# Performance work log

Hardware: AMD Instinct MI355X
Metric: run time of the kernel (lower is better)

## Reference

```python
import jax, jax.numpy as jnp
import numpy as np

MARGIN = 1.0
CONTR_LAMDA = 100.0
GN_LAMDA = 0.3
IMG_SCALE = 2
EPS = 1e-9


def bilinear(fmap, pts):
    # fmap: (B,C,H,W); pts: (B,N,2) as (x,y). Returns (B*N, C).
    B, C, H, W = fmap.shape
    N = pts.shape[1]
    x = jnp.clip(pts[..., 0], 0.0, W - 1.0)
    y = jnp.clip(pts[..., 1], 0.0, H - 1.0)
    x0 = jnp.floor(x)
    y0 = jnp.floor(y)
    wx = (x - x0)[:, None, :]
    wy = (y - y0)[:, None, :]
    x0i = x0.astype(jnp.int32)
    y0i = y0.astype(jnp.int32)
    x1i = jnp.minimum(x0i + 1, W - 1)
    y1i = jnp.minimum(y0i + 1, H - 1)
    fm = fmap.reshape(B, C, H * W)

    def gather(yi, xi):
        idx = yi * W + xi  # (B,N)
        idx = jnp.broadcast_to(idx[:, None, :], (B, C, N))
        return jnp.take_along_axis(fm, idx, axis=2)  # (B,C,N)

    v = (gather(y0i, x0i) * (1 - wx) * (1 - wy)
         + gather(y0i, x1i) * wx * (1 - wy)
         + gather(y1i, x0i) * (1 - wx) * wy
         + gather(y1i, x1i) * wx * wy)
    return v.transpose(0, 2, 1).reshape(B * N, C)


def grad2d(f):
    # central differences with edge replication (torch_gradient)
    fx = jnp.pad(f, ((0, 0), (0, 0), (0, 0), (1, 1)), mode='edge')
    gx = 0.5 * (fx[..., 2:] - fx[..., :-2])
    fy = jnp.pad(f, ((0, 0), (0, 0), (1, 1), (0, 0)), mode='edge')
    gy = 0.5 * (fy[..., 2:, :] - fy[..., :-2, :])
    return gx, gy


def gn_loss(f_t, fb, ub, noise):
    # f_t: (B*N,C); fb: (B,C,H,W); ub,noise: (B,N,2)
    B, N, _ = ub.shape
    xs = noise + ub
    f_s = bilinear(fb, xs)
    r = f_s - f_t  # (BN, C) residual
    gx, gy = grad2d(fb)
    Jx = bilinear(gx, xs)  # (BN, C)
    Jy = bilinear(gy, xs)
    # H = J^T J + eps*I  -- closed-form batched 2x2
    a = jnp.sum(Jx * Jx, axis=1) + EPS
    d = jnp.sum(Jy * Jy, axis=1) + EPS
    b = jnp.sum(Jx * Jy, axis=1)
    det = a * d - b * b
    bx = jnp.sum(Jx * r, axis=1)
    by = jnp.sum(Jy * r, axis=1)
    # Hinv @ (J^T r)
    ix = (d * bx - b * by) / det
    iy = (-b * bx + a * by) / det
    miu = xs.reshape(B * N, 2) - jnp.stack([ix, iy], axis=-1)
    du = ub.reshape(B * N, 2) - miu
    q = a * du[:, 0] ** 2 + 2.0 * b * du[:, 0] * du[:, 1] + d * du[:, 1] ** 2
    e1 = 0.5 * jnp.sum(q)
    e2 = B * N * jnp.log(jnp.asarray(2.0 * np.pi, jnp.float32)) - 0.5 * jnp.sum(jnp.log(det))
    return e1 + 2.0 * e2 / 7.0


def triplet_loss(fa_map, fb_map, ma, mb, ng):
    fa = bilinear(fa_map, ma)
    fp = bilinear(fb_map, mb)
    fn = bilinear(fb_map, ng)
    dp = jnp.linalg.norm(fa - fp, axis=1)
    dn = jnp.linalg.norm(fa - fn, axis=1)
    return jnp.mean(jax.nn.relu(dp - dn + MARGIN))


def setup_inputs() -> dict:
    key = jax.random.key(0)
    ks = jax.random.split(key, 16)
    B, C, N = 4, 32, 2048
    sizes = [64, 128, 256, 512]
    d = {}
    for i, h in enumerate(sizes):
        d[f'fa{i}'] = jax.random.normal(ks[i], (B, C, h, h), jnp.float32)
        d[f'fb{i}'] = jax.random.normal(ks[4 + i], (B, C, h, h), jnp.float32)
        d[f'noise{i}'] = jax.random.normal(ks[8 + i], (B, N, 2), jnp.float32)
    d['ma'] = jax.random.uniform(ks[12], (B, N, 2), jnp.float32) * 1024.0
    d['mb'] = jax.random.uniform(ks[13], (B, N, 2), jnp.float32) * 1024.0
    d['neg'] = jax.random.uniform(ks[14], (B, N, 2), jnp.float32) * 1024.0
    d['epoch'] = 5
    return d


def reference(fa0, fa1, fa2, fa3, fb0, fb1, fb2, fb3,
              noise0, noise1, noise2, noise3, ma, mb, neg, epoch):
    Fa = [fa0, fa1, fa2, fa3]
    Fb = [fb0, fb1, fb2, fb3]
    noises = [noise0, noise1, noise2, noise3]
    loss = jnp.float32(0.0)
    tl = jnp.float32(0.0)
    gl = jnp.float32(0.0)
    for i in range(4):
        level = 2 ** (3 - i)
        s = float(level * IMG_SCALE)
        f_t = bilinear(Fa[i], ma / s)
        lt = triplet_loss(Fa[i], Fb[i], ma / s, mb / s, neg / s)
        lg = gn_loss(f_t, Fb[i], mb / s, noises[i])
        loss = loss + CONTR_LAMDA * lt + GN_LAMDA * lg
        tl = tl + CONTR_LAMDA * lt
        gl = gl + GN_LAMDA * lg
    return loss, tl, gl
```

## Files before the change

kernel.cpp:

```cpp
#include <hip/hip_runtime.h>
#include <math.h>


struct BL { int x0, x1, y0, y1; float wx, wy; };
struct LevelPtrs { const float* fa[4]; const float* fb[4]; const float* nz[4]; };

__device__ __forceinline__ float2 load2u(const float* p) { float2 v; __builtin_memcpy(&v, p, 8); return v; }
__device__ __forceinline__ float4 load4u(const float* p) { float4 v; __builtin_memcpy(&v, p, 16); return v; }

__device__ __forceinline__ BL bl_setup2(float px, float py, int W, int H) {
    BL r;
    float x = fminf(fmaxf(px, 0.0f), (float)(W - 1));
    float y = fminf(fmaxf(py, 0.0f), (float)(H - 1));
    float fx = floorf(x), fy = floorf(y);
    r.wx = x - fx; r.wy = y - fy;
    r.x0 = (int)fx; r.y0 = (int)fy;
    if (r.x0 >= W - 1) { r.x0 = W - 2; r.wx = 1.0f; }
    if (r.y0 >= H - 1) { r.y0 = H - 2; r.wy = 1.0f; }
    r.x1 = r.x0 + 1;
    r.y1 = r.y0 + 1;
    return r;
}

__device__ __forceinline__ float bl_eval_slow(const float* __restrict__ f, int W, const BL& s) {
    float v00 = f[s.y0 * W + s.x0];
    float v01 = f[s.y0 * W + s.x1];
    float v10 = f[s.y1 * W + s.x0];
    float v11 = f[s.y1 * W + s.x1];
    float a0 = v00 + s.wx * (v01 - v00);
    float a1 = v10 + s.wx * (v11 - v10);
    return a0 + s.wy * (a1 - a0);
}

__device__ __forceinline__ void j_eval_slow(const float* __restrict__ f, int W, int H,
                                            const BL& s, float& Jx, float& Jy) {
    int xR0 = min(s.x0 + 1, W - 1), xL0 = max(s.x0 - 1, 0);
    int xR1 = min(s.x1 + 1, W - 1), xL1 = max(s.x1 - 1, 0);
    int yD0 = min(s.y0 + 1, H - 1), yU0 = max(s.y0 - 1, 0);
    int yD1 = min(s.y1 + 1, H - 1), yU1 = max(s.y1 - 1, 0);
    const float* r0 = f + s.y0 * W;
    const float* r1 = f + s.y1 * W;
    float gx00 = r0[xR0] - r0[xL0];
    float gx01 = r0[xR1] - r0[xL1];
    float gx10 = r1[xR0] - r1[xL0];
    float gx11 = r1[xR1] - r1[xL1];
    float gy00 = f[yD0 * W + s.x0] - f[yU0 * W + s.x0];
    float gy01 = f[yD0 * W + s.x1] - f[yU0 * W + s.x1];
    float gy10 = f[yD1 * W + s.x0] - f[yU1 * W + s.x0];
    float gy11 = f[yD1 * W + s.x1] - f[yU1 * W + s.x1];
    float g0 = gx00 + s.wx * (gx01 - gx00);
    float g1 = gx10 + s.wx * (gx11 - gx10);
    Jx = 0.5f * (g0 + s.wy * (g1 - g0));
    float h0 = gy00 + s.wx * (gy01 - gy00);
    float h1 = gy10 + s.wx * (gy11 - gy10);
    Jy = 0.5f * (h0 + s.wy * (h1 - h0));
}

__device__ __forceinline__ float wave64_sum(float v) {
    v += __shfl_xor(v, 32);
    v += __shfl_xor(v, 16);
    v += __shfl_xor(v, 8);
    v += __shfl_xor(v, 4);
    v += __shfl_xor(v, 2);
    v += __shfl_xor(v, 1);
    return v;
}

__device__ __forceinline__ float warp32_sum(float v) {
    v += __shfl_xor(v, 16);
    v += __shfl_xor(v, 8);
    v += __shfl_xor(v, 4);
    v += __shfl_xor(v, 2);
    v += __shfl_xor(v, 1);
    return v;
}

__global__ __launch_bounds__(1024) void sort3_kernel(
    const float* __restrict__ ma, const float* __restrict__ mb,
    const float* __restrict__ ng, int* __restrict__ perm) {
    const int cid = blockIdx.x >> 2;
    const int b = blockIdx.x & 3;
    const float* coords = (cid == 0) ? ma : (cid == 1) ? mb : ng;
    __shared__ unsigned int keys[2048];
    const float* cb = coords + (size_t)b * 2048 * 2;
    for (int i = threadIdx.x; i < 2048; i += 1024) {
        int ix = min(max((int)cb[i * 2 + 0], 0), 1023);
        int iy = min(max((int)cb[i * 2 + 1], 0), 1023);
        unsigned m = 0;
        #pragma unroll
        for (int t = 0; t < 10; ++t)
            m |= (((unsigned)(ix >> t) & 1u) << (2 * t)) | (((unsigned)(iy >> t) & 1u) << (2 * t + 1));
        keys[i] = (m << 11) | (unsigned)i;
    }
    __syncthreads();
    for (unsigned k = 2; k <= 2048; k <<= 1) {
        for (unsigned j = k >> 1; j > 0; j >>= 1) {
            unsigned t = threadIdx.x;
            unsigned i1 = 2 * t - (t & (j - 1));
            unsigned i2 = i1 + j;
            bool up = ((i1 & k) == 0);
            unsigned a = keys[i1], c = keys[i2];
            if ((a > c) == up) { keys[i1] = c; keys[i2] = a; }
            __syncthreads();
        }
    }
    for (int i = threadIdx.x; i < 2048; i += 1024)
        perm[cid * 8192 + b * 2048 + i] = (int)(keys[i] & 2047u);
}

__global__ __launch_bounds__(256) void gather_pass_kernel(
    LevelPtrs P, const float* __restrict__ ma, const float* __restrict__ ng,
    const int* __restrict__ perm, float* __restrict__ ft, float* __restrict__ fn) {
    const int bid = blockIdx.x;
    const int role = bid & 1;
    const int rest = bid >> 1;
    const int lvl = 3 - (rest >> 9);
    const int sub = rest & 511;
    const int g = sub >> 2;
    const int cq = sub & 3;
    const int tid = threadIdx.x;
    const int lane = tid & 63, w = tid >> 6;
    const int ch0 = cq * 8 + w * 2;
    const int rank = g * 64 + lane;
    const int b = rank >> 11;
    const int* pm = perm + (role ? 2 * 8192 : 0);
    const int q = (b << 11) + pm[rank];
    const int H = 64 << lvl, W = H, HW = H * W;
    const float inv_s = 0.0625f * (float)(1 << lvl);
    const float* coords = role ? ng : ma;
    const float px = coords[q * 2] * inv_s, py = coords[q * 2 + 1] * inv_s;
    BL s = bl_setup2(px, py, W, H);
    const float* src = role ? P.fb[lvl] : P.fa[lvl];
    const float* p0 = src + (size_t)(b * 32 + ch0) * HW + s.y0 * W + s.x0;
    const float* p1 = p0 + HW;

    float2 a0 = load2u(p0);
    float2 a1 = load2u(p0 + W);
    float2 c0 = load2u(p1);
    float2 c1 = load2u(p1 + W);
    __builtin_amdgcn_sched_barrier(0);
    float t0 = a0.x + s.wx * (a0.y - a0.x);
    float t1 = a1.x + s.wx * (a1.y - a1.x);
    float o0 = t0 + s.wy * (t1 - t0);
    float u0 = c0.x + s.wx * (c0.y - c0.x);
    float u1 = c1.x + s.wx * (c1.y - c1.x);
    float o1 = u0 + s.wy * (u1 - u0);

    float* dst = (role ? fn : ft) + ((size_t)lvl * 8192 + q) * 32 + ch0;
    float2 o = {o0, o1};
    *(float2*)dst = o;
}

__device__ __forceinline__ void consume_ch(
    const float* __restrict__ plane, int W, int H, const BL& sb, const BL& sx,
    bool interior, float2 m0, float2 m1,
    float4 r0, float4 r1, float4 r2, float4 r3,
    float ftv, float fnv,
    float& sp, float& sn, float& aa, float& dd, float& bb, float& bx, float& by) {
    float t0 = m0.x + sb.wx * (m0.y - m0.x);
    float t1 = m1.x + sb.wx * (m1.y - m1.x);
    float fpv = t0 + sb.wy * (t1 - t0);
    float fsv, Jx, Jy;
    if (interior) {
        float wx = sx.wx, wy = sx.wy;
        float a0 = r1.y + wx * (r1.z - r1.y);
        float a1 = r2.y + wx * (r2.z - r2.y);
        fsv = a0 + wy * (a1 - a0);
        float gx00 = r1.z - r1.x, gx01 = r1.w - r1.y;
        float gx10 = r2.z - r2.x, gx11 = r2.w - r2.y;
        float gy00 = r2.y - r0.y, gy01 = r2.z - r0.z;
        float gy10 = r3.y - r1.y, gy11 = r3.z - r1.z;
        float g0 = gx00 + wx * (gx01 - gx00);
        float g1 = gx10 + wx * (gx11 - gx10);
        Jx = 0.5f * (g0 + wy * (g1 - g0));
        float h0 = gy00 + wx * (gy01 - gy00);
        float h1 = gy10 + wx * (gy11 - gy10);
        Jy = 0.5f * (h0 + wy * (h1 - h0));
    } else {
        fsv = bl_eval_slow(plane, W, sx);
        j_eval_slow(plane, W, H, sx, Jx, Jy);
    }
    float rr = fsv - ftv;
    float dp = ftv - fpv, dn = ftv - fnv;
    sp += dp * dp;
    sn += dn * dn;
    aa += Jx * Jx;
    dd += Jy * Jy;
    bb += Jx * Jy;
    bx += Jx * rr;
    by += Jy * rr;
}

__global__ __launch_bounds__(256) void gn_main_kernel(
    LevelPtrs P, const float* __restrict__ mb, const int* __restrict__ perm_mb,
    const float* __restrict__ ft, const float* __restrict__ fn,
    float* __restrict__ blk_out) {
    const int bid = blockIdx.x;
    const int lvl = 3 - (bid >> 7);
    const int g = bid & 127;
    const int tid = threadIdx.x;
    const int lane = tid & 63, w = tid >> 6, ch0 = w * 8;
    const int rank = g * 64 + lane;
    const int b = rank >> 11;
    const int q = (b << 11) + perm_mb[rank];
    const int H = 64 << lvl, W = H, HW = H * W;
    const float inv_s = 0.0625f * (float)(1 << lvl);
    const float* noise = P.nz[lvl];
    const int p2 = q * 2;
    const float nzx = noise[p2], nzy = noise[p2 + 1];
    const float pbx = mb[p2] * inv_s, pby = mb[p2 + 1] * inv_s;
    const float xsx = nzx + pbx, xsy = nzy + pby;
    BL sb = bl_setup2(pbx, pby, W, H);
    BL sx = bl_setup2(xsx, xsy, W, H);
    const bool interior = (sx.x0 >= 1) & (sx.x0 <= W - 3) & (sx.y0 >= 1) & (sx.y0 <= H - 3);
    const int pbx0 = min(max(sx.x0 - 1, 0), W - 4);
    const int pby0 = min(max(sx.y0 - 1, 0), H - 4);
    const float* fb0 = P.fb[lvl] + (size_t)(b * 32 + ch0) * HW;

    const float* ftp = ft + ((size_t)lvl * 8192 + q) * 32 + ch0;
    const float* fnp = fn + ((size_t)lvl * 8192 + q) * 32 + ch0;
    float4 ftA = *(const float4*)ftp, ftB = *(const float4*)(ftp + 4);
    float4 fnA = *(const float4*)fnp, fnB = *(const float4*)(fnp + 4);
    float ftv[8] = {ftA.x, ftA.y, ftA.z, ftA.w, ftB.x, ftB.y, ftB.z, ftB.w};
    float fnv[8] = {fnA.x, fnA.y, fnA.z, fnA.w, fnB.x, fnB.y, fnB.z, fnB.w};

    float sp = 0, sn = 0, aa = 0, dd = 0, bb = 0, bx = 0, by = 0;
    const int mboff0 = sb.y0 * W + sb.x0;
    const int pboff = pby0 * W + pbx0;
    #pragma unroll
    for (int cc = 0; cc < 8; cc += 2) {
        const float* p0 = fb0 + (size_t)cc * HW;
        const float* p1 = p0 + HW;
        float2 m00 = load2u(p0 + mboff0);
        float2 m01 = load2u(p0 + mboff0 + W);
        float2 m10 = load2u(p1 + mboff0);
        float2 m11 = load2u(p1 + mboff0 + W);
        const float* xb0 = p0 + pboff;
        const float* xb1 = p1 + pboff;
        float4 r00 = load4u(xb0), r01 = load4u(xb0 + W), r02 = load4u(xb0 + 2 * W), r03 = load4u(xb0 + 3 * W);
        float4 r10 = load4u(xb1), r11 = load4u(xb1 + W), r12 = load4u(xb1 + 2 * W), r13 = load4u(xb1 + 3 * W);
        consume_ch(p0, W, H, sb, sx, interior, m00, m01, r00, r01, r02, r03,
                   ftv[cc], fnv[cc], sp, sn, aa, dd, bb, bx, by);
        consume_ch(p1, W, H, sb, sx, interior, m10, m11, r10, r11, r12, r13,
                   ftv[cc + 1], fnv[cc + 1], sp, sn, aa, dd, bb, bx, by);
    }

    __shared__ float red[4][64][7];
    red[w][lane][0] = sp; red[w][lane][1] = sn; red[w][lane][2] = aa;
    red[w][lane][3] = dd; red[w][lane][4] = bb; red[w][lane][5] = bx;
    red[w][lane][6] = by;
    __syncthreads();
    if (tid < 64) {
        float t[7];
        #pragma unroll
        for (int k = 0; k < 7; ++k)
            t[k] = red[0][tid][k] + red[1][tid][k] + red[2][tid][k] + red[3][tid][k];
        float a2 = t[2] + 1e-9f, d2 = t[3] + 1e-9f, b2 = t[4];
        float det = a2 * d2 - b2 * b2;
        float ix = (d2 * t[5] - b2 * t[6]) / det;
        float iy = (a2 * t[6] - b2 * t[5]) / det;
        float dux = ix - nzx;
        float duy = iy - nzy;
        float qv = a2 * dux * dux + 2.0f * b2 * dux * duy + d2 * duy * duy;
        float trip = fmaxf(sqrtf(t[0]) - sqrtf(t[1]) + 1.0f, 0.0f);
        float ld = logf(det);
        trip = wave64_sum(trip);
        qv = wave64_sum(qv);
        ld = wave64_sum(ld);
        if (tid == 0) {
            blk_out[bid * 3 + 0] = trip;
            blk_out[bid * 3 + 1] = qv;
            blk_out[bid * 3 + 2] = ld;
        }
    }
}

__global__ __launch_bounds__(256) void gn_final_kernel(
    const float* __restrict__ part, int nblk, float* __restrict__ out) {
    __shared__ double sd[3][256];
    double st = 0.0, sq = 0.0, sl = 0.0;
    for (int i = threadIdx.x; i < nblk; i += 256) {
        st += (double)part[i * 3 + 0];
        sq += (double)part[i * 3 + 1];
        sl += (double)part[i * 3 + 2];
    }
    sd[0][threadIdx.x] = st; sd[1][threadIdx.x] = sq; sd[2][threadIdx.x] = sl;
    __syncthreads();
    for (int s = 128; s > 0; s >>= 1) {
        if (threadIdx.x < s) {
            sd[0][threadIdx.x] += sd[0][threadIdx.x + s];
            sd[1][threadIdx.x] += sd[1][threadIdx.x + s];
            sd[2][threadIdx.x] += sd[2][threadIdx.x + s];
        }
        __syncthreads();
    }
    if (threadIdx.x == 0) {
        double S_t = sd[0][0], S_q = sd[1][0], S_l = sd[2][0];
        double tl = 100.0 * S_t / 8192.0;
        double e2 = 4.0 * 8192.0 * 1.8378770664093453 - 0.5 * S_l;
        double gl = 0.3 * (0.5 * S_q + (2.0 / 7.0) * e2);
        out[0] = (float)(tl + gl);
        out[1] = (float)tl;
        out[2] = (float)gl;
    }
}

struct Task {
    const float* fac;
    const float* fbc;
    BL sa, sb, sg, sx;
    float nzx, nzy;
    bool fast;
    float2 va0, va1, vb0, vb1, vg0, vg1;
    float4 xm, x0, x1, x2;
    float fav, fpv, fnv, fsv, Jx, Jy;
};

__device__ __forceinline__ void task_setup(Task& T, int rank, const LevelPtrs& P,
                                           int lvl, int c, int W, int H, float inv_s,
                                           const float* __restrict__ ma,
                                           const float* __restrict__ mb,
                                           const float* __restrict__ ng) {
    const int b = rank >> 11;
    const int q = rank;
    const int HW = H * W;
    T.fac = P.fa[lvl] + (size_t)(b * 32 + c) * HW;
    T.fbc = P.fb[lvl] + (size_t)(b * 32 + c) * HW;
    const float* noise = P.nz[lvl];
    const int p2 = q * 2;
    T.nzx = noise[p2]; T.nzy = noise[p2 + 1];
    const float pax = ma[p2] * inv_s, pay = ma[p2 + 1] * inv_s;
    const float pbx = mb[p2] * inv_s, pby = mb[p2 + 1] * inv_s;
    const float pnx = ng[p2] * inv_s, pny = ng[p2 + 1] * inv_s;
    const float xsx = T.nzx + pbx, xsy = T.nzy + pby;
    T.sa = bl_setup2(pax, pay, W, H);
    T.sb = bl_setup2(pbx, pby, W, H);
    T.sg = bl_setup2(pnx, pny, W, H);
    T.sx = bl_setup2(xsx, xsy, W, H);
    T.fast = (T.sx.x0 >= 1) & (T.sx.x0 <= W - 3) & (T.sx.y0 >= 1) & (T.sx.y0 <= H - 3);
}

__device__ __forceinline__ void task_issue(Task& T, int W, int H) {
    T.va0 = load2u(T.fac + T.sa.y0 * W + T.sa.x0);
    T.va1 = load2u(T.fac + T.sa.y1 * W + T.sa.x0);
    T.vb0 = load2u(T.fbc + T.sb.y0 * W + T.sb.x0);
    T.vb1 = load2u(T.fbc + T.sb.y1 * W + T.sb.x0);
    T.vg0 = load2u(T.fbc + T.sg.y0 * W + T.sg.x0);
    T.vg1 = load2u(T.fbc + T.sg.y1 * W + T.sg.x0);
    int bx0 = min(max(T.sx.x0 - 1, 0), W - 4);
    int by0 = min(max(T.sx.y0 - 1, 0), H - 4);
    const float* xbp = T.fbc + by0 * W + bx0;
    T.xm = load4u(xbp);
    T.x0 = load4u(xbp + W);
    T.x1 = load4u(xbp + 2 * W);
    T.x2 = load4u(xbp + 3 * W);
}

__device__ __forceinline__ void task_consume(Task& T, int W, int H) {
    {
        float t0 = T.va0.x + T.sa.wx * (T.va0.y - T.va0.x);
        float t1 = T.va1.x + T.sa.wx * (T.va1.y - T.va1.x);
        T.fav = t0 + T.sa.wy * (t1 - t0);
    }
    {
        float t0 = T.vb0.x + T.sb.wx * (T.vb0.y - T.vb0.x);
        float t1 = T.vb1.x + T.sb.wx * (T.vb1.y - T.vb1.x);
        T.fpv = t0 + T.sb.wy * (t1 - t0);
    }
    {
        float t0 = T.vg0.x + T.sg.wx * (T.vg0.y - T.vg0.x);
        float t1 = T.vg1.x + T.sg.wx * (T.vg1.y - T.vg1.x);
        T.fnv = t0 + T.sg.wy * (t1 - t0);
    }
    if (T.fast) {
        float wx = T.sx.wx, wy = T.sx.wy;
        float t0 = T.x0.y + wx * (T.x0.z - T.x0.y);
        float t1 = T.x1.y + wx * (T.x1.z - T.x1.y);
        T.fsv = t0 + wy * (t1 - t0);
        float gx00 = T.x0.z - T.x0.x, gx01 = T.x0.w - T.x0.y;
        float gx10 = T.x1.z - T.x1.x, gx11 = T.x1.w - T.x1.y;
        float gy00 = T.x1.y - T.xm.y, gy01 = T.x1.z - T.xm.z;
        float gy10 = T.x2.y - T.x0.y, gy11 = T.x2.z - T.x0.z;
        float g0 = gx00 + wx * (gx01 - gx00);
        float g1 = gx10 + wx * (gx11 - gx10);
        T.Jx = 0.5f * (g0 + wy * (g1 - g0));
        float h0 = gy00 + wx * (gy01 - gy00);
        float h1 = gy10 + wx * (gy11 - gy10);
        T.Jy = 0.5f * (h0 + wy * (h1 - h0));
    } else {
        T.fsv = bl_eval_slow(T.fbc, W, T.sx);
        j_eval_slow(T.fbc, W, H, T.sx, T.Jx, T.Jy);
    }
}

__device__ __forceinline__ void task_reduce(const Task& T, int c, float* red0,
                                            float* red1, float* red2, int slot2) {
    float r = T.fsv - T.fav;
    float a  = warp32_sum(T.Jx * T.Jx);
    float dd = warp32_sum(T.Jy * T.Jy);
    float bb = warp32_sum(T.Jx * T.Jy);
    float bx = warp32_sum(T.Jx * r);
    float by = warp32_sum(T.Jy * r);
    float dfp = T.fav - T.fpv, dfn = T.fav - T.fnv;
    float sp = warp32_sum(dfp * dfp);
    float sn = warp32_sum(dfn * dfn);
    if (c == 0) {
        a += 1e-9f; dd += 1e-9f;
        float det = a * dd - bb * bb;
        float ix = (dd * bx - bb * by) / det;
        float iy = (a * by - bb * bx) / det;
        float dux = ix - T.nzx;
        float duy = iy - T.nzy;
        float qv = a * dux * dux + 2.0f * bb * dux * duy + dd * duy * duy;
        red0[slot2] = fmaxf(sqrtf(sp) - sqrtf(sn) + 1.0f, 0.0f);
        red1[slot2] = qv;
        red2[slot2] = logf(det);
    }
}

__global__ __launch_bounds__(256) void gn_fallback_kernel(
    LevelPtrs P, const float* __restrict__ ma, const float* __restrict__ mb,
    const float* __restrict__ ng, float* __restrict__ blk_out) {
    const int tid = threadIdx.x;
    const int c = tid & 31;
    const int slot = tid >> 5;
    const int lvl = slot >> 1;
    const int po = slot & 1;
    const int bid = blockIdx.x;
    const int base = bid * 4;
    const int H = 64 << lvl;
    const int W = H;
    const float inv_s = 0.0625f * (float)(1 << lvl);

    Task T0, T1;
    task_setup(T0, base + po,     P, lvl, c, W, H, inv_s, ma, mb, ng);
    task_setup(T1, base + 2 + po, P, lvl, c, W, H, inv_s, ma, mb, ng);
    task_issue(T0, W, H);
    task_issue(T1, W, H);
    task_consume(T0, W, H);
    task_consume(T1, W, H);

    __shared__ float red[3][16];
    task_reduce(T0, c, red[0], red[1], red[2], slot * 2 + 0);
    task_reduce(T1, c, red[0], red[1], red[2], slot * 2 + 1);
    __syncthreads();
    if (tid == 0) {
        float t = 0.0f, qq = 0.0f, l = 0.0f;
        #pragma unroll
        for (int i = 0; i < 16; ++i) { t += red[0][i]; qq += red[1][i]; l += red[2][i]; }
        blk_out[bid * 3 + 0] = t;
        blk_out[bid * 3 + 1] = qq;
        blk_out[bid * 3 + 2] = l;
    }
}

extern "C" void kernel_launch(void* const* d_in, const int* in_sizes, int n_in,
                              void* d_out, int out_size, void* d_ws, size_t ws_size,
                              hipStream_t stream) {
    const bool dict_order = (in_sizes[1] == in_sizes[0]);
    LevelPtrs P;
    for (int i = 0; i < 4; ++i) {
        if (dict_order) {
            P.fa[i] = (const float*)d_in[3 * i + 0];
            P.fb[i] = (const float*)d_in[3 * i + 1];
            P.nz[i] = (const float*)d_in[3 * i + 2];
        } else {
            P.fa[i] = (const float*)d_in[i];
            P.fb[i] = (const float*)d_in[4 + i];
            P.nz[i] = (const float*)d_in[8 + i];
        }
    }
    const float* ma = (const float*)d_in[12];
    const float* mb = (const float*)d_in[13];
    const float* ng = (const float*)d_in[14];

    float* ws = (float*)d_ws;
    const size_t FT_OFF = 26112;
    const size_t FN_OFF = FT_OFF + 4 * 8192 * 32;
    const size_t NEED = (FN_OFF + 4 * 8192 * 32) * 4;

    if (ws_size >= NEED) {
        float* partials = ws;
        int* perm = (int*)(ws + 1536);
        float* ft = ws + FT_OFF;
        float* fn = ws + FN_OFF;
        sort3_kernel<<<12, 1024, 0, stream>>>(ma, mb, ng, perm);
        gather_pass_kernel<<<4096, 256, 0, stream>>>(P, ma, ng, perm, ft, fn);
        gn_main_kernel<<<512, 256, 0, stream>>>(P, mb, perm + 8192, ft, fn, partials);
        gn_final_kernel<<<1, 256, 0, stream>>>(partials, 512, (float*)d_out);
    } else {
        float* partials = ws;
        gn_fallback_kernel<<<2048, 256, 0, stream>>>(P, ma, mb, ng, partials);
        gn_final_kernel<<<1, 256, 0, stream>>>(partials, 2048, (float*)d_out);
    }
}
```

Measured before the change: 92.22 us.

## Fuse anchor and negative gathers into main GN kernel, drop gather pass

```diff
diff --git a/kernel.cpp b/kernel.cpp
--- a/kernel.cpp
+++ b/kernel.cpp
@@ -20,6 +20,12 @@
     r.x1 = r.x0 + 1;
     r.y1 = r.y0 + 1;
     return r;
+}
+
+__device__ __forceinline__ float bl_lerp(float2 r0, float2 r1, const BL& s) {
+    float t0 = r0.x + s.wx * (r0.y - r0.x);
+    float t1 = r1.x + s.wx * (r1.y - r1.x);
+    return t0 + s.wy * (t1 - t0);
 }
 
 __device__ __forceinline__ float bl_eval_slow(const float* __restrict__ f, int W, const BL& s) {
@@ -75,14 +81,11 @@
     return v;
 }
 
-__global__ __launch_bounds__(1024) void sort3_kernel(
-    const float* __restrict__ ma, const float* __restrict__ mb,
-    const float* __restrict__ ng, int* __restrict__ perm) {
-    const int cid = blockIdx.x >> 2;
-    const int b = blockIdx.x & 3;
-    const float* coords = (cid == 0) ? ma : (cid == 1) ? mb : ng;
+__global__ __launch_bounds__(1024) void sort_mb_kernel(
+    const float* __restrict__ mb, int* __restrict__ perm) {
+    const int b = blockIdx.x;
     __shared__ unsigned int keys[2048];
-    const float* cb = coords + (size_t)b * 2048 * 2;
+    const float* cb = mb + (size_t)b * 2048 * 2;
     for (int i = threadIdx.x; i < 2048; i += 1024) {
         int ix = min(max((int)cb[i * 2 + 0], 0), 1023);
         int iy = min(max((int)cb[i * 2 + 1], 0), 1023);
@@ -105,61 +108,18 @@
         }
     }
     for (int i = threadIdx.x; i < 2048; i += 1024)
-        perm[cid * 8192 + b * 2048 + i] = (int)(keys[i] & 2047u);
-}
-
-__global__ __launch_bounds__(256) void gather_pass_kernel(
-    LevelPtrs P, const float* __restrict__ ma, const float* __restrict__ ng,
-    const int* __restrict__ perm, float* __restrict__ ft, float* __restrict__ fn) {
-    const int bid = blockIdx.x;
-    const int role = bid & 1;
-    const int rest = bid >> 1;
-    const int lvl = 3 - (rest >> 9);
-    const int sub = rest & 511;
-    const int g = sub >> 2;
-    const int cq = sub & 3;
-    const int tid = threadIdx.x;
-    const int lane = tid & 63, w = tid >> 6;
-    const int ch0 = cq * 8 + w * 2;
-    const int rank = g * 64 + lane;
-    const int b = rank >> 11;
-    const int* pm = perm + (role ? 2 * 8192 : 0);
-    const int q = (b << 11) + pm[rank];
-    const int H = 64 << lvl, W = H, HW = H * W;
-    const float inv_s = 0.0625f * (float)(1 << lvl);
-    const float* coords = role ? ng : ma;
-    const float px = coords[q * 2] * inv_s, py = coords[q * 2 + 1] * inv_s;
-    BL s = bl_setup2(px, py, W, H);
-    const float* src = role ? P.fb[lvl] : P.fa[lvl];
-    const float* p0 = src + (size_t)(b * 32 + ch0) * HW + s.y0 * W + s.x0;
-    const float* p1 = p0 + HW;
-
-    float2 a0 = load2u(p0);
-    float2 a1 = load2u(p0 + W);
-    float2 c0 = load2u(p1);
-    float2 c1 = load2u(p1 + W);
-    __builtin_amdgcn_sched_barrier(0);
-    float t0 = a0.x + s.wx * (a0.y - a0.x);
-    float t1 = a1.x + s.wx * (a1.y - a1.x);
-    float o0 = t0 + s.wy * (t1 - t0);
-    float u0 = c0.x + s.wx * (c0.y - c0.x);
-    float u1 = c1.x + s.wx * (c1.y - c1.x);
-    float o1 = u0 + s.wy * (u1 - u0);
-
-    float* dst = (role ? fn : ft) + ((size_t)lvl * 8192 + q) * 32 + ch0;
-    float2 o = {o0, o1};
-    *(float2*)dst = o;
-}
-
-__device__ __forceinline__ void consume_ch(
-    const float* __restrict__ plane, int W, int H, const BL& sb, const BL& sx,
-    bool interior, float2 m0, float2 m1,
+        perm[b * 2048 + i] = (int)(keys[i] & 2047u);
+}
+
+__device__ __forceinline__ void consume_ch2(
+    const float* __restrict__ plane, int W, int H,
+    const BL& sa, const BL& sb, const BL& sg, const BL& sx, bool interior,
+    float2 va0, float2 va1, float2 m0, float2 m1, float2 g0v, float2 g1v,
     float4 r0, float4 r1, float4 r2, float4 r3,
-    float ftv, float fnv,
     float& sp, float& sn, float& aa, float& dd, float& bb, float& bx, float& by) {
-    float t0 = m0.x + sb.wx * (m0.y - m0.x);
-    float t1 = m1.x + sb.wx * (m1.y - m1.x);
-    float fpv = t0 + sb.wy * (t1 - t0);
+    float fav = bl_lerp(va0, va1, sa);
+    float fpv = bl_lerp(m0, m1, sb);
+    float fnv = bl_lerp(g0v, g1v, sg);
     float fsv, Jx, Jy;
     if (interior) {
         float wx = sx.wx, wy = sx.wy;
@@ -180,8 +140,8 @@
         fsv = bl_eval_slow(plane, W, sx);
         j_eval_slow(plane, W, H, sx, Jx, Jy);
     }
-    float rr = fsv - ftv;
-    float dp = ftv - fpv, dn = ftv - fnv;
+    float rr = fsv - fav;
+    float dp = fav - fpv, dn = fav - fnv;
     sp += dp * dp;
     sn += dn * dn;
     aa += Jx * Jx;
@@ -191,9 +151,9 @@
     by += Jy * rr;
 }
 
-__global__ __launch_bounds__(256) void gn_main_kernel(
-    LevelPtrs P, const float* __restrict__ mb, const int* __restrict__ perm_mb,
-    const float* __restrict__ ft, const float* __restrict__ fn,
+__global__ __launch_bounds__(256) void gn_fused_kernel(
+    LevelPtrs P, const float* __restrict__ ma, const float* __restrict__ mb,
+    const float* __restrict__ ng, const int* __restrict__ perm_mb,
     float* __restrict__ blk_out) {
     const int bid = blockIdx.x;
     const int lvl = 3 - (bid >> 7);
@@ -208,41 +168,53 @@
     const float* noise = P.nz[lvl];
     const int p2 = q * 2;
     const float nzx = noise[p2], nzy = noise[p2 + 1];
+    const float pax = ma[p2] * inv_s, pay = ma[p2 + 1] * inv_s;
     const float pbx = mb[p2] * inv_s, pby = mb[p2 + 1] * inv_s;
+    const float pnx = ng[p2] * inv_s, pny = ng[p2 + 1] * inv_s;
     const float xsx = nzx + pbx, xsy = nzy + pby;
+    BL sa = bl_setup2(pax, pay, W, H);
     BL sb = bl_setup2(pbx, pby, W, H);
+    BL sg = bl_setup2(pnx, pny, W, H);
     BL sx = bl_setup2(xsx, xsy, W, H);
     const bool interior = (sx.x0 >= 1) & (sx.x0 <= W - 3) & (sx.y0 >= 1) & (sx.y0 <= H - 3);
     const int pbx0 = min(max(sx.x0 - 1, 0), W - 4);
     const int pby0 = min(max(sx.y0 - 1, 0), H - 4);
+    const float* fa0 = P.fa[lvl] + (size_t)(b * 32 + ch0) * HW;
     const float* fb0 = P.fb[lvl] + (size_t)(b * 32 + ch0) * HW;
-
-    const float* ftp = ft + ((size_t)lvl * 8192 + q) * 32 + ch0;
-    const float* fnp = fn + ((size_t)lvl * 8192 + q) * 32 + ch0;
-    float4 ftA = *(const float4*)ftp, ftB = *(const float4*)(ftp + 4);
-    float4 fnA = *(const float4*)fnp, fnB = *(const float4*)(fnp + 4);
-    float ftv[8] = {ftA.x, ftA.y, ftA.z, ftA.w, ftB.x, ftB.y, ftB.z, ftB.w};
-    float fnv[8] = {fnA.x, fnA.y, fnA.z, fnA.w, fnB.x, fnB.y, fnB.z, fnB.w};
+    const int maoff = sa.y0 * W + sa.x0;
+    const int mboff = sb.y0 * W + sb.x0;
+    const int ngoff = sg.y0 * W + sg.x0;
+    const int pboff = pby0 * W + pbx0;
 
     float sp = 0, sn = 0, aa = 0, dd = 0, bb = 0, bx = 0, by = 0;
-    const int mboff0 = sb.y0 * W + sb.x0;
-    const int pboff = pby0 * W + pbx0;
     #pragma unroll
     for (int cc = 0; cc < 8; cc += 2) {
-        const float* p0 = fb0 + (size_t)cc * HW;
-        const float* p1 = p0 + HW;
-        float2 m00 = load2u(p0 + mboff0);
-        float2 m01 = load2u(p0 + mboff0 + W);
-        float2 m10 = load2u(p1 + mboff0);
-        float2 m11 = load2u(p1 + mboff0 + W);
-        const float* xb0 = p0 + pboff;
-        const float* xb1 = p1 + pboff;
+        const float* a0p = fa0 + (size_t)cc * HW;
+        const float* a1p = a0p + HW;
+        const float* b0p = fb0 + (size_t)cc * HW;
+        const float* b1p = b0p + HW;
+        float2 va00 = load2u(a0p + maoff);
+        float2 va01 = load2u(a0p + maoff + W);
+        float2 va10 = load2u(a1p + maoff);
+        float2 va11 = load2u(a1p + maoff + W);
+        float2 m00 = load2u(b0p + mboff);
+        float2 m01 = load2u(b0p + mboff + W);
+        float2 m10 = load2u(b1p + mboff);
+        float2 m11 = load2u(b1p + mboff + W);
+        float2 g00 = load2u(b0p + ngoff);
+        float2 g01 = load2u(b0p + ngoff + W);
+        float2 g10 = load2u(b1p + ngoff);
+        float2 g11 = load2u(b1p + ngoff + W);
+        const float* xb0 = b0p + pboff;
+        const float* xb1 = b1p + pboff;
         float4 r00 = load4u(xb0), r01 = load4u(xb0 + W), r02 = load4u(xb0 + 2 * W), r03 = load4u(xb0 + 3 * W);
         float4 r10 = load4u(xb1), r11 = load4u(xb1 + W), r12 = load4u(xb1 + 2 * W), r13 = load4u(xb1 + 3 * W);
-        consume_ch(p0, W, H, sb, sx, interior, m00, m01, r00, r01, r02, r03,
-                   ftv[cc], fnv[cc], sp, sn, aa, dd, bb, bx, by);
-        consume_ch(p1, W, H, sb, sx, interior, m10, m11, r10, r11, r12, r13,
-                   ftv[cc + 1], fnv[cc + 1], sp, sn, aa, dd, bb, bx, by);
+        consume_ch2(b0p, W, H, sa, sb, sg, sx, interior,
+                    va00, va01, m00, m01, g00, g01, r00, r01, r02, r03,
+                    sp, sn, aa, dd, bb, bx, by);
+        consume_ch2(b1p, W, H, sa, sb, sg, sx, interior,
+                    va10, va11, m10, m11, g10, g11, r10, r11, r12, r13,
+                    sp, sn, aa, dd, bb, bx, by);
     }
 
     __shared__ float red[4][64][7];
@@ -259,8 +231,12 @@
         float det = a2 * d2 - b2 * b2;
         float ix = (d2 * t[5] - b2 * t[6]) / det;
         float iy = (a2 * t[6] - b2 * t[5]) / det;
-        float dux = ix - nzx;
-        float duy = iy - nzy;
+        const int rank2 = g * 64 + tid;
+        const int b2i = rank2 >> 11;
+        const int q2 = (b2i << 11) + perm_mb[rank2];
+        const float nz2x = noise[q2 * 2], nz2y = noise[q2 * 2 + 1];
+        float dux = ix - nz2x;
+        float duy = iy - nz2y;
         float qv = a2 * dux * dux + 2.0f * b2 * dux * duy + d2 * duy * duy;
         float trip = fmaxf(sqrtf(t[0]) - sqrtf(t[1]) + 1.0f, 0.0f);
         float ld = logf(det);
@@ -475,18 +451,13 @@
     const float* ng = (const float*)d_in[14];
 
     float* ws = (float*)d_ws;
-    const size_t FT_OFF = 26112;
-    const size_t FN_OFF = FT_OFF + 4 * 8192 * 32;
-    const size_t NEED = (FN_OFF + 4 * 8192 * 32) * 4;
+    const size_t NEED = (1536 + 8192) * 4;
 
     if (ws_size >= NEED) {
         float* partials = ws;
         int* perm = (int*)(ws + 1536);
-        float* ft = ws + FT_OFF;
-        float* fn = ws + FN_OFF;
-        sort3_kernel<<<12, 1024, 0, stream>>>(ma, mb, ng, perm);
-        gather_pass_kernel<<<4096, 256, 0, stream>>>(P, ma, ng, perm, ft, fn);
-        gn_main_kernel<<<512, 256, 0, stream>>>(P, mb, perm + 8192, ft, fn, partials);
+        sort_mb_kernel<<<4, 1024, 0, stream>>>(mb, perm);
+        gn_fused_kernel<<<512, 256, 0, stream>>>(P, ma, mb, ng, perm, partials);
         gn_final_kernel<<<1, 256, 0, stream>>>(partials, 512, (float*)d_out);
     } else {
         float* partials = ws;
```

Result: slower. 111.8 us (+21.2%).
